# Kernel optimization log

Hardware: AMD Instinct MI355X
Metric: run time of the kernel (lower is better)

The kernel has to match this reference:

```python
import jax, jax.numpy as jnp
import numpy as np

D = 1024      # latent_dimension
NH = 8        # num_heads
ND = 256      # drug num_functions
NT = 128      # target num_functions
B = 128       # batch
EPS_LN = 1e-5
EPS_COS = 1e-8


def _proj_attend(x, W, b, in_w, in_b, out_w, out_b, g, beta):
    """ParallelFcWithAttention.forward: per-feature Linear(1,D)+ReLU, MHSA, LN, sum.
    x: (B, >=F); W,b: (F, D); in_w: (3D, D); out_w: (D, D); g,beta: (D,)."""
    F = W.shape[0]
    # fused batched scale+bias+ReLU replacing the Python loop of Linear(1,D)
    h = jax.nn.relu(x[:, :F, None] * W[None] + b[None])           # (B, F, D)
    Bsz = h.shape[0]
    qkv = h @ in_w.T + in_b                                       # (B, F, 3D)
    q, k, v = jnp.split(qkv, 3, axis=-1)
    Dh = D // NH
    def split_heads(t):
        return t.reshape(Bsz, F, NH, Dh).transpose(0, 2, 1, 3)   # (B, H, F, Dh)
    q, k, v = split_heads(q), split_heads(k), split_heads(v)
    scale = np.float32(1.0 / np.sqrt(Dh))
    scores = jnp.einsum('bhqd,bhkd->bhqk', q, k) * scale          # (B, H, F, F)
    attn = jax.nn.softmax(scores, axis=-1)
    o = jnp.einsum('bhqk,bhkd->bhqd', attn, v)                    # (B, H, F, Dh)
    o = o.transpose(0, 2, 1, 3).reshape(Bsz, F, D)
    o = o @ out_w.T + out_b
    mu = o.mean(axis=-1, keepdims=True)
    var = ((o - mu) ** 2).mean(axis=-1, keepdims=True)
    o = (o - mu) / jnp.sqrt(var + EPS_LN) * g + beta              # LayerNorm
    return o.sum(axis=1)                                          # (B, D)


def setup_inputs() -> dict:
    key = jax.random.key(0)
    ks = jax.random.split(key, 20)
    s = np.float32(0.02)
    inp = {
        'drug':    jax.random.normal(ks[0], (B, 2048), jnp.float32),
        'target':  jax.random.normal(ks[1], (B, 1024), jnp.float32),
        'dW':      jax.random.normal(ks[2], (ND, D), jnp.float32) * s,
        'db':      jax.random.normal(ks[3], (ND, D), jnp.float32) * s,
        'd_in_w':  jax.random.normal(ks[4], (3 * D, D), jnp.float32) * s,
        'd_in_b':  jnp.zeros((3 * D,), jnp.float32),
        'd_out_w': jax.random.normal(ks[5], (D, D), jnp.float32) * s,
        'd_out_b': jnp.zeros((D,), jnp.float32),
        'd_g':     jnp.ones((D,), jnp.float32),
        'd_beta':  jnp.zeros((D,), jnp.float32),
        'tW':      jax.random.normal(ks[6], (NT, D), jnp.float32) * s,
        'tb':      jax.random.normal(ks[7], (NT, D), jnp.float32) * s,
        't_in_w':  jax.random.normal(ks[8], (3 * D, D), jnp.float32) * s,
        't_in_b':  jnp.zeros((3 * D,), jnp.float32),
        't_out_w': jax.random.normal(ks[9], (D, D), jnp.float32) * s,
        't_out_b': jnp.zeros((D,), jnp.float32),
        't_g':     jnp.ones((D,), jnp.float32),
        't_beta':  jnp.zeros((D,), jnp.float32),
    }
    return inp


def reference(drug, target, dW, db, d_in_w, d_in_b, d_out_w, d_out_b, d_g, d_beta,
              tW, tb, t_in_w, t_in_b, t_out_w, t_out_b, t_g, t_beta):
    dp = _proj_attend(drug, dW, db, d_in_w, d_in_b, d_out_w, d_out_b, d_g, d_beta)   # (B, D)
    tp = _proj_attend(target, tW, tb, t_in_w, t_in_b, t_out_w, t_out_b, t_g, t_beta) # (B, D)
    # Cosine similarity over latent dim (torch CosineSimilarity dim=1), then sigmoid
    dot = jnp.sum(dp * tp, axis=-1)
    denom = jnp.maximum(jnp.linalg.norm(dp, axis=-1) * jnp.linalg.norm(tp, axis=-1), EPS_COS)
    return jax.nn.sigmoid(dot / denom)                                               # (B,)
```

## Files before the change

kernel.cpp:

```cpp
#include <hip/hip_runtime.h>

typedef unsigned short u16;
typedef unsigned int   u32;
typedef unsigned char  u8;

using bf16x8 = __attribute__((ext_vector_type(8))) short;
using f32x4  = __attribute__((ext_vector_type(4))) float;
using i32x4  = __attribute__((ext_vector_type(4))) int;

__device__ __forceinline__ float bf2f(u16 h) {
  u32 u = ((u32)h) << 16;
  return __builtin_bit_cast(float, u);
}
__device__ __forceinline__ u16 f2bf(float f) {
  u32 u = __builtin_bit_cast(u32, f);
  u += 0x7fffu + ((u >> 16) & 1u);
  return (u16)(u >> 16);
}

__device__ __forceinline__ void gload16(const void* src, void* ldsdst) {
  __builtin_amdgcn_global_load_lds(
      (const __attribute__((address_space(1))) void*)src,
      (__attribute__((address_space(3))) void*)ldsdst, 16, 0, 0);
}

__device__ __forceinline__ void mfma_i8(i32x4& c, i32x4 a, i32x4 b) {
  asm volatile("v_mfma_i32_16x16x64_i8 %0, %1, %2, %0" : "+a"(c) : "v"(a), "v"(b));
}

__device__ __forceinline__ int xcd_swz(int wg, int nwg) {
  int q = nwg >> 3, r = nwg & 7, xcd = wg & 7, loc = wg >> 3;
  return (xcd < r ? xcd * (q + 1) : r * (q + 1) + (xcd - r) * q) + loc;
}

__global__ __launch_bounds__(256) void cvt_bf16(const float* __restrict__ in,
                                                u16* __restrict__ out, int n8) {
  int i = blockIdx.x * 256 + threadIdx.x;
  if (i >= n8) return;
  const float* p = in + (size_t)i * 8;
  bf16x8 o;
#pragma unroll
  for (int j = 0; j < 8; ++j) o[j] = (short)f2bf(p[j]);
  *(bf16x8*)(out + (size_t)i * 8) = o;
}

__global__ __launch_bounds__(256) void cvt_w_i8(const float* __restrict__ in,
                                                u8* __restrict__ out,
                                                float* __restrict__ sc) {
  const int row  = blockIdx.x * 4 + (threadIdx.x >> 6);
  const int lane = threadIdx.x & 63;
  const float4* p = (const float4*)(in + (size_t)row * 1024 + lane * 16);
  float v[16];
  float mx = 0.f;
#pragma unroll
  for (int i = 0; i < 4; ++i) {
    float4 t = p[i];
    v[i * 4 + 0] = t.x; v[i * 4 + 1] = t.y; v[i * 4 + 2] = t.z; v[i * 4 + 3] = t.w;
#pragma unroll
    for (int j = 0; j < 4; ++j) mx = fmaxf(mx, fabsf(v[i * 4 + j]));
  }
#pragma unroll
  for (int m = 1; m < 64; m <<= 1) mx = fmaxf(mx, __shfl_xor(mx, m));
  const float scale = mx > 0.f ? 127.f / mx : 0.f;
  u32 pk[4];
#pragma unroll
  for (int i = 0; i < 4; ++i) {
    u32 b0 = (u32)(__float2int_rn(v[i * 4 + 0] * scale) & 0xff);
    u32 b1 = (u32)(__float2int_rn(v[i * 4 + 1] * scale) & 0xff);
    u32 b2 = (u32)(__float2int_rn(v[i * 4 + 2] * scale) & 0xff);
    u32 b3 = (u32)(__float2int_rn(v[i * 4 + 3] * scale) & 0xff);
    pk[i] = b0 | (b1 << 8) | (b2 << 16) | (b3 << 24);
  }
  *(uint4*)(out + (size_t)row * 1024 + lane * 16) = make_uint4(pk[0], pk[1], pk[2], pk[3]);
  if (lane == 0) sc[row] = mx > 0.f ? mx / 127.f : 0.f;
}

__global__ __launch_bounds__(256) void hgen_i8(const float* __restrict__ x,
                                               const float* __restrict__ W,
                                               const float* __restrict__ bias,
                                               u8* __restrict__ h, float* __restrict__ hsc,
                                               int F, int logF, int b0, int xstride) {
  const int row  = blockIdx.x * 4 + (threadIdx.x >> 6);
  const int lane = threadIdx.x & 63;
  const int f = row & (F - 1);
  const int b = b0 + (row >> logF);
  const float xv = x[(size_t)b * xstride + f];
  const float4* wp = (const float4*)(W + (size_t)f * 1024 + lane * 16);
  const float4* bp = (const float4*)(bias + (size_t)f * 1024 + lane * 16);
  float hv[16];
  float mx = 0.f;
#pragma unroll
  for (int i = 0; i < 4; ++i) {
    float4 wv = wp[i];
    float4 bv = bp[i];
    hv[i * 4 + 0] = fmaxf(xv * wv.x + bv.x, 0.f);
    hv[i * 4 + 1] = fmaxf(xv * wv.y + bv.y, 0.f);
    hv[i * 4 + 2] = fmaxf(xv * wv.z + bv.z, 0.f);
    hv[i * 4 + 3] = fmaxf(xv * wv.w + bv.w, 0.f);
#pragma unroll
    for (int j = 0; j < 4; ++j) mx = fmaxf(mx, hv[i * 4 + j]);
  }
#pragma unroll
  for (int m = 1; m < 64; m <<= 1) mx = fmaxf(mx, __shfl_xor(mx, m));
  const float scale = mx > 0.f ? 127.f / mx : 0.f;
  u32 pk[4];
#pragma unroll
  for (int i = 0; i < 4; ++i) {
    u32 q0 = (u32)__float2int_rn(hv[i * 4 + 0] * scale);
    u32 q1 = (u32)__float2int_rn(hv[i * 4 + 1] * scale);
    u32 q2 = (u32)__float2int_rn(hv[i * 4 + 2] * scale);
    u32 q3 = (u32)__float2int_rn(hv[i * 4 + 3] * scale);
    pk[i] = q0 | (q1 << 8) | (q2 << 16) | (q3 << 24);
  }
  *(uint4*)(h + (size_t)row * 1024 + lane * 16) = make_uint4(pk[0], pk[1], pk[2], pk[3]);
  if (lane == 0) hsc[row] = mx > 0.f ? mx / 127.f : 0.f;
}

__global__ __launch_bounds__(512, 4) void gemm_i8(const u8* __restrict__ A,
                                                  const u8* __restrict__ B,
                                                  const float* __restrict__ sAsc,
                                                  const float* __restrict__ sBsc,
                                                  const float* __restrict__ bias,
                                                  u16* __restrict__ C,
                                                  int M, int N, int K) {
  __shared__ u8 sA[3][256 * 64];
  __shared__ u8 sB[3][128 * 64];
  const int tid  = threadIdx.x;
  const int lane = tid & 63;
  const int w    = tid >> 6;
  const int wm   = w >> 1;
  const int wn   = w & 1;

  const int nwg = gridDim.x * gridDim.y;
  const int wg  = blockIdx.y * gridDim.x + blockIdx.x;
  const int swz = xcd_swz(wg, nwg);
  const int n0 = (swz % gridDim.x) * 128;
  const int m0 = (swz / gridDim.x) * 256;

  i32x4 acc[4][4] = {};

  const int r_in  = lane >> 2;
  const int s_src = (lane & 3) ^ ((lane >> 3) & 3);

  auto stage = [&](int kt, int b) {
    const int k0 = kt << 6;
    gload16(A + (size_t)(m0 + w * 16 + r_in) * K + k0 + s_src * 16, &sA[b][w * 1024]);
    gload16(A + (size_t)(m0 + (w + 8) * 16 + r_in) * K + k0 + s_src * 16, &sA[b][(w + 8) * 1024]);
    gload16(B + (size_t)(n0 + w * 16 + r_in) * K + k0 + s_src * 16, &sB[b][w * 1024]);
  };

  const int NT = K >> 6;
  stage(0, 0);
  stage(1, 1);
  asm volatile("s_waitcnt vmcnt(3)" ::: "memory");
  __builtin_amdgcn_s_barrier();

  int cur = 0, nx = 2;
  for (int t = 0; t < NT; ++t) {
    const bool more = (t + 2 < NT);
    if (more) stage(t + 2, nx);

    i32x4 af[4], bg[4];
    const int g = lane >> 4;
#pragma unroll
    for (int mf = 0; mf < 4; ++mf) {
      int ra = wm * 64 + mf * 16 + (lane & 15);
      af[mf] = *(const i32x4*)(&sA[cur][ra * 64 + ((g ^ ((ra >> 1) & 3)) * 16)]);
    }
#pragma unroll
    for (int nf = 0; nf < 4; ++nf) {
      int rb = wn * 64 + nf * 16 + (lane & 15);
      bg[nf] = *(const i32x4*)(&sB[cur][rb * 64 + ((g ^ ((rb >> 1) & 3)) * 16)]);
    }
    asm volatile("s_waitcnt lgkmcnt(0)" ::: "memory");
    __builtin_amdgcn_sched_barrier(0);
    __builtin_amdgcn_s_setprio(1);
#pragma unroll
    for (int mf = 0; mf < 4; ++mf)
#pragma unroll
      for (int nf = 0; nf < 4; ++nf)
        mfma_i8(acc[mf][nf], af[mf], bg[nf]);
    __builtin_amdgcn_s_setprio(0);
    if (more) asm volatile("s_waitcnt vmcnt(3)" ::: "memory");
    else      asm volatile("s_waitcnt vmcnt(0)" ::: "memory");
    __builtin_amdgcn_s_barrier();
    cur = (cur == 2) ? 0 : cur + 1;
    nx  = (nx  == 2) ? 0 : nx  + 1;
  }

#pragma unroll
  for (int nf = 0; nf < 4; ++nf) {
    int cl = n0 + wn * 64 + nf * 16 + (lane & 15);
    float sb  = sBsc[cl];
    float bsv = bias[cl];
#pragma unroll
    for (int mf = 0; mf < 4; ++mf) {
      int r0 = m0 + wm * 64 + mf * 16 + (lane >> 4) * 4;
      float4 sa4 = *(const float4*)(sAsc + r0);
      const float* sap = (const float*)&sa4;
#pragma unroll
      for (int reg = 0; reg < 4; ++reg)
        C[(size_t)(r0 + reg) * N + cl] =
            f2bf((float)acc[mf][nf][reg] * (sap[reg] * sb) + bsv);
    }
  }
}

__global__ __launch_bounds__(512, 4) void gemm_ph(const u16* __restrict__ A,
                                                  const u16* __restrict__ B,
                                                  const float* __restrict__ bias,
                                                  u16* __restrict__ C,
                                                  int M, int N, int K) {
  __shared__ u16 sA[3][256 * 32];
  __shared__ u16 sB[3][128 * 32];
  const int tid  = threadIdx.x;
  const int lane = tid & 63;
  const int w    = tid >> 6;
  const int wm   = w >> 1;
  const int wn   = w & 1;

  const int nwg = gridDim.x * gridDim.y;
  const int wg  = blockIdx.y * gridDim.x + blockIdx.x;
  const int swz = xcd_swz(wg, nwg);
  const int n0 = (swz % gridDim.x) * 128;
  const int m0 = (swz / gridDim.x) * 256;

  f32x4 acc[4][4] = {};

  const int r_in  = lane >> 2;
  const int s_src = (lane & 3) ^ ((lane >> 3) & 3);

  auto stage = [&](int kt, int b) {
    const int k0 = kt << 5;
    gload16(A + (size_t)(m0 + w * 16 + r_in) * K + k0 + s_src * 8, &sA[b][w * 512]);
    gload16(A + (size_t)(m0 + (w + 8) * 16 + r_in) * K + k0 + s_src * 8, &sA[b][(w + 8) * 512]);
    gload16(B + (size_t)(n0 + w * 16 + r_in) * K + k0 + s_src * 8, &sB[b][w * 512]);
  };

  const int NT = K >> 5;
  stage(0, 0);
  stage(1, 1);
  asm volatile("s_waitcnt vmcnt(3)" ::: "memory");
  __builtin_amdgcn_s_barrier();

  int cur = 0, nx = 2;
  for (int t = 0; t < NT; ++t) {
    const bool more = (t + 2 < NT);
    if (more) stage(t + 2, nx);

    bf16x8 af[4], bg[4];
    const int g = lane >> 4;
#pragma unroll
    for (int mf = 0; mf < 4; ++mf) {
      int ra = wm * 64 + mf * 16 + (lane & 15);
      af[mf] = *(const bf16x8*)(&sA[cur][ra * 32 + ((g ^ ((ra >> 1) & 3)) * 8)]);
    }
#pragma unroll
    for (int nf = 0; nf < 4; ++nf) {
      int rb = wn * 64 + nf * 16 + (lane & 15);
      bg[nf] = *(const bf16x8*)(&sB[cur][rb * 32 + ((g ^ ((rb >> 1) & 3)) * 8)]);
    }
    asm volatile("s_waitcnt lgkmcnt(0)" ::: "memory");
    __builtin_amdgcn_sched_barrier(0);
    __builtin_amdgcn_s_setprio(1);
#pragma unroll
    for (int mf = 0; mf < 4; ++mf)
#pragma unroll
      for (int nf = 0; nf < 4; ++nf)
        acc[mf][nf] = __builtin_amdgcn_mfma_f32_16x16x32_bf16(af[mf], bg[nf], acc[mf][nf], 0, 0, 0);
    __builtin_amdgcn_s_setprio(0);
    if (more) asm volatile("s_waitcnt vmcnt(3)" ::: "memory");
    else      asm volatile("s_waitcnt vmcnt(0)" ::: "memory");
    __builtin_amdgcn_s_barrier();
    cur = (cur == 2) ? 0 : cur + 1;
    nx  = (nx  == 2) ? 0 : nx  + 1;
  }

#pragma unroll
  for (int nf = 0; nf < 4; ++nf) {
    int cl = n0 + wn * 64 + nf * 16 + (lane & 15);
    float bsv = bias[cl];
#pragma unroll
    for (int mf = 0; mf < 4; ++mf) {
      int r0 = m0 + wm * 64 + mf * 16 + (lane >> 4) * 4;
#pragma unroll
      for (int reg = 0; reg < 4; ++reg)
        C[(size_t)(r0 + reg) * N + cl] = f2bf(acc[mf][nf][reg] + bsv);
    }
  }
}

__global__ __launch_bounds__(512) void attn(const u16* __restrict__ qkv,
                                            u16* __restrict__ o_out, int F) {
  __shared__ u16 q_lds[128 * 136];
  __shared__ u16 k_lds[64 * 136];
  __shared__ u16 vT[128 * 72];
  __shared__ u16 p_lds[8 * 16 * 72];

  const int tid  = threadIdx.x;
  const int lane = tid & 63;
  const int w    = tid >> 6;

  const int swzb = xcd_swz(blockIdx.x, gridDim.x);
  const int nqb  = F >> 7;
  const int qb   = swzb % nqb;
  const int head = (swzb / nqb) & 7;
  const int bc   = swzb / (nqb * 8);

  const size_t rowbase = (size_t)bc * F * 3072;
  const float scale = 0.08838834764831845f;

  {
    const u16* qsrc = qkv + rowbase + (size_t)(qb * 128) * 3072 + head * 128;
    for (int it = tid; it < 2048; it += 512) {
      int r = it >> 4, s = it & 15;
      bf16x8 v = *(const bf16x8*)(qsrc + (size_t)r * 3072 + s * 8);
      bf16x8 o;
#pragma unroll
      for (int j = 0; j < 8; ++j) o[j] = (short)f2bf(bf2f((u16)v[j]) * scale);
      *(bf16x8*)(q_lds + r * 136 + s * 8) = o;
    }
  }

  f32x4 o_acc[8] = {};
  float m_run = -INFINITY, l_run = 0.f;
  const int qr = lane & 15;
  const int g4 = lane >> 4;

  const int nkb = F >> 6;
  for (int kb = 0; kb < nkb; ++kb) {
    __syncthreads();
    const u16* ksrc = qkv + rowbase + (size_t)(kb * 64) * 3072 + 1024 + head * 128;
    const u16* vsrc = ksrc + 1024;
    for (int it = tid; it < 1024; it += 512) {
      int r = it >> 4, s = it & 15;
      *(bf16x8*)(k_lds + r * 136 + s * 8) = *(const bf16x8*)(ksrc + (size_t)r * 3072 + s * 8);
    }
    {
      int g2 = tid >> 4, s = tid & 15;
      const u16* v0 = vsrc + (size_t)(2 * g2) * 3072 + s * 8;
      bf16x8 a = *(const bf16x8*)(v0);
      bf16x8 b = *(const bf16x8*)(v0 + 3072);
      int rs0 = (2 * g2) ^ ((s & 7) << 3);
      int d0  = s * 8;
#pragma unroll
      for (int j = 0; j < 8; ++j) {
        u32 pk = (u32)(u16)a[j] | ((u32)(u16)b[j] << 16);
        *(u32*)(vT + (d0 + j) * 72 + rs0) = pk;
      }
    }
    __syncthreads();

    f32x4 sa[4] = {};
#pragma unroll
    for (int kk = 0; kk < 4; ++kk) {
      bf16x8 bq = *(const bf16x8*)(q_lds + (w * 16 + qr) * 136 + kk * 32 + 8 * g4);
#pragma unroll
      for (int f = 0; f < 4; ++f) {
        bf16x8 ak = *(const bf16x8*)(k_lds + (f * 16 + qr) * 136 + kk * 32 + 8 * g4);
        sa[f] = __builtin_amdgcn_mfma_f32_16x16x32_bf16(ak, bq, sa[f], 0, 0, 0);
      }
    }

    float tmax = -INFINITY;
#pragma unroll
    for (int f = 0; f < 4; ++f)
#pragma unroll
      for (int rr = 0; rr < 4; ++rr) tmax = fmaxf(tmax, sa[f][rr]);
    tmax = fmaxf(tmax, __shfl_xor(tmax, 16));
    tmax = fmaxf(tmax, __shfl_xor(tmax, 32));
    float mnew  = fmaxf(m_run, tmax);
    float alpha = __expf(m_run - mnew);
    float psum  = 0.f;
#pragma unroll
    for (int f = 0; f < 4; ++f) {
      u16 pp[4];
#pragma unroll
      for (int rr = 0; rr < 4; ++rr) {
        float p = __expf(sa[f][rr] - mnew);
        psum += p;
        pp[rr] = f2bf(p);
      }
      uint2 u;
      u.x = (u32)pp[0] | ((u32)pp[1] << 16);
      u.y = (u32)pp[2] | ((u32)pp[3] << 16);
      *(uint2*)(p_lds + w * 1152 + qr * 72 + f * 16 + g4 * 4) = u;
    }
    psum += __shfl_xor(psum, 16);
    psum += __shfl_xor(psum, 32);
    l_run = l_run * alpha + psum;
    m_run = mnew;

#pragma unroll
    for (int rr = 0; rr < 4; ++rr) {
      float ar = __shfl(alpha, g4 * 4 + rr);
#pragma unroll
      for (int g = 0; g < 8; ++g) o_acc[g][rr] *= ar;
    }

#pragma unroll
    for (int kk2 = 0; kk2 < 2; ++kk2) {
      bf16x8 pa = *(const bf16x8*)(p_lds + w * 1152 + qr * 72 + kk2 * 32 + 8 * g4);
#pragma unroll
      for (int g = 0; g < 8; ++g) {
        int swv = ((g * 2 + (qr >> 3)) & 7) << 3;
        bf16x8 vb = *(const bf16x8*)(vT + (g * 16 + qr) * 72 + ((kk2 * 32 + 8 * g4) ^ swv));
        o_acc[g] = __builtin_amdgcn_mfma_f32_16x16x32_bf16(pa, vb, o_acc[g], 0, 0, 0);
      }
    }
  }

  float linv = 1.f / l_run;
#pragma unroll
  for (int rr = 0; rr < 4; ++rr) {
    float lr = __shfl(linv, g4 * 4 + rr);
    size_t row = (size_t)bc * F + qb * 128 + w * 16 + g4 * 4 + rr;
#pragma unroll
    for (int g = 0; g < 8; ++g)
      o_out[row * 1024 + head * 128 + g * 16 + qr] = f2bf(o_acc[g][rr] * lr);
  }
}

__global__ __launch_bounds__(256) void ln_stats(const u16* __restrict__ proj,
                                                float2* __restrict__ stats) {
  int row  = blockIdx.x * 4 + (threadIdx.x >> 6);
  int lane = threadIdx.x & 63;
  const u16* p = proj + (size_t)row * 1024;
  float s = 0.f, s2 = 0.f;
#pragma unroll
  for (int i = 0; i < 2; ++i) {
    bf16x8 v = *(const bf16x8*)(p + (lane + i * 64) * 8);
#pragma unroll
    for (int j = 0; j < 8; ++j) { float f = bf2f((u16)v[j]); s += f; s2 += f * f; }
  }
#pragma unroll
  for (int m = 1; m < 64; m <<= 1) { s += __shfl_xor(s, m); s2 += __shfl_xor(s2, m); }
  if (lane == 0) {
    float mu  = s * (1.f / 1024.f);
    float var = s2 * (1.f / 1024.f) - mu * mu;
    stats[row] = make_float2(mu, rsqrtf(var + 1e-5f));
  }
}

__global__ __launch_bounds__(256) void ln_accum(const u16* __restrict__ proj,
                                                const float2* __restrict__ stats,
                                                const float* __restrict__ g,
                                                const float* __restrict__ beta,
                                                float* __restrict__ dp, int F, int b0) {
  int d  = blockIdx.x * 256 + threadIdx.x;
  int bc = blockIdx.z;
  int f0 = blockIdx.y * 64;
  const u16* base = proj + ((size_t)(bc * F + f0)) * 1024 + d;
  const float2* st = stats + bc * F + f0;
  float acc = 0.f;
  for (int f = 0; f < 64; ++f) {
    float2 s = st[f];
    acc += (bf2f(base[(size_t)f * 1024]) - s.x) * s.y;
  }
  acc = acc * g[d] + 64.f * beta[d];
  atomicAdd(&dp[(size_t)(b0 + bc) * 1024 + d], acc);
}

__global__ __launch_bounds__(256) void cosine_sig(const float* __restrict__ dp,
                                                  const float* __restrict__ tp,
                                                  float* __restrict__ out) {
  __shared__ float red[3][4];
  int b = blockIdx.x;
  int tid = threadIdx.x, lane = tid & 63, w = tid >> 6;
  float dot = 0.f, n1 = 0.f, n2 = 0.f;
  for (int i = tid; i < 1024; i += 256) {
    float a = dp[(size_t)b * 1024 + i], c = tp[(size_t)b * 1024 + i];
    dot += a * c; n1 += a * a; n2 += c * c;
  }
#pragma unroll
  for (int m = 1; m < 64; m <<= 1) {
    dot += __shfl_xor(dot, m); n1 += __shfl_xor(n1, m); n2 += __shfl_xor(n2, m);
  }
  if (lane == 0) { red[0][w] = dot; red[1][w] = n1; red[2][w] = n2; }
  __syncthreads();
  if (tid == 0) {
    dot = red[0][0] + red[0][1] + red[0][2] + red[0][3];
    n1  = red[1][0] + red[1][1] + red[1][2] + red[1][3];
    n2  = red[2][0] + red[2][1] + red[2][2] + red[2][3];
    float denom = fmaxf(sqrtf(n1) * sqrtf(n2), 1e-8f);
    out[b] = 1.f / (1.f + __expf(-dot / denom));
  }
}

extern "C" void kernel_launch(void* const* d_in, const int* in_sizes, int n_in,
                              void* d_out, int out_size, void* d_ws, size_t ws_size,
                              hipStream_t stream) {
  const float* drug   = (const float*)d_in[0];
  const float* target = (const float*)d_in[1];

  char* p = (char*)d_ws;
  auto alloc = [&](size_t bytes) -> char* {
    char* r = p; p += (bytes + 255) & ~(size_t)255; return r;
  };

  u8*    w8_d   = (u8*)alloc((size_t)3072 * 1024);
  float* wsc_d  = (float*)alloc((size_t)3072 * 4);
  u8*    w8_t   = (u8*)alloc((size_t)3072 * 1024);
  float* wsc_t  = (float*)alloc((size_t)3072 * 4);
  u16*   w_out_d = (u16*)alloc((size_t)1024 * 1024 * 2);
  u16*   w_out_t = (u16*)alloc((size_t)1024 * 1024 * 2);
  float* dp    = (float*)alloc((size_t)2 * 128 * 1024 * 4);
  float* tp    = dp + 128 * 1024;

  size_t fixed = (size_t)(p - (char*)d_ws);
  size_t per = (size_t)256 * 1024
             + (size_t)256 * 4
             + (size_t)256 * 3072 * 2
             + (size_t)256 * 1024 * 2 * 2
             + (size_t)256 * 8 + 4096;
  int Bc = 8;
  if      (fixed + 128 * per <= ws_size) Bc = 128;
  else if (fixed +  64 * per <= ws_size) Bc = 64;
  else if (fixed +  32 * per <= ws_size) Bc = 32;
  else if (fixed +  16 * per <= ws_size) Bc = 16;

  u8*    h8     = (u8*)alloc((size_t)Bc * 256 * 1024);
  float* hsc    = (float*)alloc((size_t)Bc * 256 * 4);
  u16*   qkvbuf = (u16*)alloc((size_t)Bc * 256 * 3072 * 2);
  u16*   obuf   = (u16*)alloc((size_t)Bc * 256 * 1024 * 2);
  u16*   projbuf= (u16*)alloc((size_t)Bc * 256 * 1024 * 2);
  float2* statsb = (float2*)alloc((size_t)Bc * 256 * 8);

  cvt_w_i8<<<768, 256, 0, stream>>>((const float*)d_in[4],  w8_d, wsc_d);
  cvt_w_i8<<<768, 256, 0, stream>>>((const float*)d_in[12], w8_t, wsc_t);
  cvt_bf16<<<512, 256, 0, stream>>>((const float*)d_in[6],  w_out_d, 1024 * 128);
  cvt_bf16<<<512, 256, 0, stream>>>((const float*)d_in[14], w_out_t, 1024 * 128);
  hipMemsetAsync(dp, 0, (size_t)2 * 128 * 1024 * 4, stream);

  for (int br = 0; br < 2; ++br) {
    const int F = br ? 128 : 256, logF = br ? 7 : 8, xstride = br ? 1024 : 2048;
    const float* x    = br ? target : drug;
    const float* W    = (const float*)d_in[br ? 10 : 2];
    const float* Wb   = (const float*)d_in[br ? 11 : 3];
    u8*          w8   = br ? w8_t : w8_d;
    float*       wsc  = br ? wsc_t : wsc_d;
    const float* inb  = (const float*)d_in[br ? 13 : 5];
    u16*         wout = br ? w_out_t : w_out_d;
    const float* outb = (const float*)d_in[br ? 15 : 7];
    const float* gg   = (const float*)d_in[br ? 16 : 8];
    const float* bb   = (const float*)d_in[br ? 17 : 9];
    float*       accp = br ? tp : dp;

    const int nb = (br ? (2 * Bc > 128 ? 128 : 2 * Bc) : (Bc > 128 ? 128 : Bc));

    for (int b0 = 0; b0 < 128; b0 += nb) {
      const int Mr = nb * F;
      hgen_i8<<<Mr / 4, 256, 0, stream>>>(x, W, Wb, h8, hsc, F, logF, b0, xstride);
      gemm_i8<<<dim3(3072 / 128, Mr / 256), 512, 0, stream>>>(h8, w8, hsc, wsc, inb, qkvbuf, Mr, 3072, 1024);
      attn<<<(F / 128) * 8 * nb, 512, 0, stream>>>(qkvbuf, obuf, F);
      gemm_ph<<<dim3(1024 / 128, Mr / 256), 512, 0, stream>>>(obuf, wout, outb, projbuf, Mr, 1024, 1024);
      ln_stats<<<Mr / 4, 256, 0, stream>>>(projbuf, statsb);
      ln_accum<<<dim3(4, F / 64, nb), 256, 0, stream>>>(projbuf, statsb, gg, bb, accp, F, b0);
    }
  }
  cosine_sig<<<128, 256, 0, stream>>>(dp, tp, (float*)d_out);
}
```

Measured before the change: 618.9 us.

## Quantize out-projection to int8 GEMM and keep Q fragments in registers

```diff
diff --git a/kernel.cpp b/kernel.cpp
--- a/kernel.cpp
+++ b/kernel.cpp
@@ -31,17 +31,6 @@
 __device__ __forceinline__ int xcd_swz(int wg, int nwg) {
   int q = nwg >> 3, r = nwg & 7, xcd = wg & 7, loc = wg >> 3;
   return (xcd < r ? xcd * (q + 1) : r * (q + 1) + (xcd - r) * q) + loc;
-}
-
-__global__ __launch_bounds__(256) void cvt_bf16(const float* __restrict__ in,
-                                                u16* __restrict__ out, int n8) {
-  int i = blockIdx.x * 256 + threadIdx.x;
-  if (i >= n8) return;
-  const float* p = in + (size_t)i * 8;
-  bf16x8 o;
-#pragma unroll
-  for (int j = 0; j < 8; ++j) o[j] = (short)f2bf(p[j]);
-  *(bf16x8*)(out + (size_t)i * 8) = o;
 }
 
 __global__ __launch_bounds__(256) void cvt_w_i8(const float* __restrict__ in,
@@ -58,6 +47,40 @@
     v[i * 4 + 0] = t.x; v[i * 4 + 1] = t.y; v[i * 4 + 2] = t.z; v[i * 4 + 3] = t.w;
 #pragma unroll
     for (int j = 0; j < 4; ++j) mx = fmaxf(mx, fabsf(v[i * 4 + j]));
+  }
+#pragma unroll
+  for (int m = 1; m < 64; m <<= 1) mx = fmaxf(mx, __shfl_xor(mx, m));
+  const float scale = mx > 0.f ? 127.f / mx : 0.f;
+  u32 pk[4];
+#pragma unroll
+  for (int i = 0; i < 4; ++i) {
+    u32 b0 = (u32)(__float2int_rn(v[i * 4 + 0] * scale) & 0xff);
+    u32 b1 = (u32)(__float2int_rn(v[i * 4 + 1] * scale) & 0xff);
+    u32 b2 = (u32)(__float2int_rn(v[i * 4 + 2] * scale) & 0xff);
+    u32 b3 = (u32)(__float2int_rn(v[i * 4 + 3] * scale) & 0xff);
+    pk[i] = b0 | (b1 << 8) | (b2 << 16) | (b3 << 24);
+  }
+  *(uint4*)(out + (size_t)row * 1024 + lane * 16) = make_uint4(pk[0], pk[1], pk[2], pk[3]);
+  if (lane == 0) sc[row] = mx > 0.f ? mx / 127.f : 0.f;
+}
+
+__global__ __launch_bounds__(256) void quant_i8(const u16* __restrict__ in,
+                                                u8* __restrict__ out,
+                                                float* __restrict__ sc) {
+  const int row  = blockIdx.x * 4 + (threadIdx.x >> 6);
+  const int lane = threadIdx.x & 63;
+  const u16* p = in + (size_t)row * 1024 + lane * 16;
+  float v[16];
+  float mx = 0.f;
+#pragma unroll
+  for (int i = 0; i < 2; ++i) {
+    bf16x8 t = *(const bf16x8*)(p + i * 8);
+#pragma unroll
+    for (int j = 0; j < 8; ++j) {
+      float f = bf2f((u16)t[j]);
+      v[i * 8 + j] = f;
+      mx = fmaxf(mx, fabsf(f));
+    }
   }
 #pragma unroll
   for (int m = 1; m < 64; m <<= 1) mx = fmaxf(mx, __shfl_xor(mx, m));
@@ -206,93 +229,8 @@
   }
 }
 
-__global__ __launch_bounds__(512, 4) void gemm_ph(const u16* __restrict__ A,
-                                                  const u16* __restrict__ B,
-                                                  const float* __restrict__ bias,
-                                                  u16* __restrict__ C,
-                                                  int M, int N, int K) {
-  __shared__ u16 sA[3][256 * 32];
-  __shared__ u16 sB[3][128 * 32];
-  const int tid  = threadIdx.x;
-  const int lane = tid & 63;
-  const int w    = tid >> 6;
-  const int wm   = w >> 1;
-  const int wn   = w & 1;
-
-  const int nwg = gridDim.x * gridDim.y;
-  const int wg  = blockIdx.y * gridDim.x + blockIdx.x;
-  const int swz = xcd_swz(wg, nwg);
-  const int n0 = (swz % gridDim.x) * 128;
-  const int m0 = (swz / gridDim.x) * 256;
-
-  f32x4 acc[4][4] = {};
-
-  const int r_in  = lane >> 2;
-  const int s_src = (lane & 3) ^ ((lane >> 3) & 3);
-
-  auto stage = [&](int kt, int b) {
-    const int k0 = kt << 5;
-    gload16(A + (size_t)(m0 + w * 16 + r_in) * K + k0 + s_src * 8, &sA[b][w * 512]);
-    gload16(A + (size_t)(m0 + (w + 8) * 16 + r_in) * K + k0 + s_src * 8, &sA[b][(w + 8) * 512]);
-    gload16(B + (size_t)(n0 + w * 16 + r_in) * K + k0 + s_src * 8, &sB[b][w * 512]);
-  };
-
-  const int NT = K >> 5;
-  stage(0, 0);
-  stage(1, 1);
-  asm volatile("s_waitcnt vmcnt(3)" ::: "memory");
-  __builtin_amdgcn_s_barrier();
-
-  int cur = 0, nx = 2;
-  for (int t = 0; t < NT; ++t) {
-    const bool more = (t + 2 < NT);
-    if (more) stage(t + 2, nx);
-
-    bf16x8 af[4], bg[4];
-    const int g = lane >> 4;
-#pragma unroll
-    for (int mf = 0; mf < 4; ++mf) {
-      int ra = wm * 64 + mf * 16 + (lane & 15);
-      af[mf] = *(const bf16x8*)(&sA[cur][ra * 32 + ((g ^ ((ra >> 1) & 3)) * 8)]);
-    }
-#pragma unroll
-    for (int nf = 0; nf < 4; ++nf) {
-      int rb = wn * 64 + nf * 16 + (lane & 15);
-      bg[nf] = *(const bf16x8*)(&sB[cur][rb * 32 + ((g ^ ((rb >> 1) & 3)) * 8)]);
-    }
-    asm volatile("s_waitcnt lgkmcnt(0)" ::: "memory");
-    __builtin_amdgcn_sched_barrier(0);
-    __builtin_amdgcn_s_setprio(1);
-#pragma unroll
-    for (int mf = 0; mf < 4; ++mf)
-#pragma unroll
-      for (int nf = 0; nf < 4; ++nf)
-        acc[mf][nf] = __builtin_amdgcn_mfma_f32_16x16x32_bf16(af[mf], bg[nf], acc[mf][nf], 0, 0, 0);
-    __builtin_amdgcn_s_setprio(0);
-    if (more) asm volatile("s_waitcnt vmcnt(3)" ::: "memory");
-    else      asm volatile("s_waitcnt vmcnt(0)" ::: "memory");
-    __builtin_amdgcn_s_barrier();
-    cur = (cur == 2) ? 0 : cur + 1;
-    nx  = (nx  == 2) ? 0 : nx  + 1;
-  }
-
-#pragma unroll
-  for (int nf = 0; nf < 4; ++nf) {
-    int cl = n0 + wn * 64 + nf * 16 + (lane & 15);
-    float bsv = bias[cl];
-#pragma unroll
-    for (int mf = 0; mf < 4; ++mf) {
-      int r0 = m0 + wm * 64 + mf * 16 + (lane >> 4) * 4;
-#pragma unroll
-      for (int reg = 0; reg < 4; ++reg)
-        C[(size_t)(r0 + reg) * N + cl] = f2bf(acc[mf][nf][reg] + bsv);
-    }
-  }
-}
-
-__global__ __launch_bounds__(512) void attn(const u16* __restrict__ qkv,
-                                            u16* __restrict__ o_out, int F) {
-  __shared__ u16 q_lds[128 * 136];
+__global__ __launch_bounds__(512, 4) void attn(const u16* __restrict__ qkv,
+                                               u16* __restrict__ o_out, int F) {
   __shared__ u16 k_lds[64 * 136];
   __shared__ u16 vT[128 * 72];
   __shared__ u16 p_lds[8 * 16 * 72];
@@ -310,22 +248,24 @@
   const size_t rowbase = (size_t)bc * F * 3072;
   const float scale = 0.08838834764831845f;
 
+  const int qr = lane & 15;
+  const int g4 = lane >> 4;
+
+  bf16x8 qreg[4];
   {
-    const u16* qsrc = qkv + rowbase + (size_t)(qb * 128) * 3072 + head * 128;
-    for (int it = tid; it < 2048; it += 512) {
-      int r = it >> 4, s = it & 15;
-      bf16x8 v = *(const bf16x8*)(qsrc + (size_t)r * 3072 + s * 8);
-      bf16x8 o;
-#pragma unroll
-      for (int j = 0; j < 8; ++j) o[j] = (short)f2bf(bf2f((u16)v[j]) * scale);
-      *(bf16x8*)(q_lds + r * 136 + s * 8) = o;
+    const u16* qsrc = qkv + rowbase +
+                      (size_t)(qb * 128 + w * 16 + qr) * 3072 + head * 128;
+#pragma unroll
+    for (int kk = 0; kk < 4; ++kk) {
+      bf16x8 v = *(const bf16x8*)(qsrc + kk * 32 + 8 * g4);
+#pragma unroll
+      for (int j = 0; j < 8; ++j) v[j] = (short)f2bf(bf2f((u16)v[j]) * scale);
+      qreg[kk] = v;
     }
   }
 
   f32x4 o_acc[8] = {};
   float m_run = -INFINITY, l_run = 0.f;
-  const int qr = lane & 15;
-  const int g4 = lane >> 4;
 
   const int nkb = F >> 6;
   for (int kb = 0; kb < nkb; ++kb) {
@@ -354,11 +294,10 @@
     f32x4 sa[4] = {};
 #pragma unroll
     for (int kk = 0; kk < 4; ++kk) {
-      bf16x8 bq = *(const bf16x8*)(q_lds + (w * 16 + qr) * 136 + kk * 32 + 8 * g4);
 #pragma unroll
       for (int f = 0; f < 4; ++f) {
         bf16x8 ak = *(const bf16x8*)(k_lds + (f * 16 + qr) * 136 + kk * 32 + 8 * g4);
-        sa[f] = __builtin_amdgcn_mfma_f32_16x16x32_bf16(ak, bq, sa[f], 0, 0, 0);
+        sa[f] = __builtin_amdgcn_mfma_f32_16x16x32_bf16(ak, qreg[kk], sa[f], 0, 0, 0);
       }
     }
 
@@ -498,14 +437,16 @@
     char* r = p; p += (bytes + 255) & ~(size_t)255; return r;
   };
 
-  u8*    w8_d   = (u8*)alloc((size_t)3072 * 1024);
-  float* wsc_d  = (float*)alloc((size_t)3072 * 4);
-  u8*    w8_t   = (u8*)alloc((size_t)3072 * 1024);
-  float* wsc_t  = (float*)alloc((size_t)3072 * 4);
-  u16*   w_out_d = (u16*)alloc((size_t)1024 * 1024 * 2);
-  u16*   w_out_t = (u16*)alloc((size_t)1024 * 1024 * 2);
-  float* dp    = (float*)alloc((size_t)2 * 128 * 1024 * 4);
-  float* tp    = dp + 128 * 1024;
+  u8*    w8_d    = (u8*)alloc((size_t)3072 * 1024);
+  float* wsc_d   = (float*)alloc((size_t)3072 * 4);
+  u8*    w8_t    = (u8*)alloc((size_t)3072 * 1024);
+  float* wsc_t   = (float*)alloc((size_t)3072 * 4);
+  u8*    w8o_d   = (u8*)alloc((size_t)1024 * 1024);
+  float* wsco_d  = (float*)alloc((size_t)1024 * 4);
+  u8*    w8o_t   = (u8*)alloc((size_t)1024 * 1024);
+  float* wsco_t  = (float*)alloc((size_t)1024 * 4);
+  float* dp      = (float*)alloc((size_t)2 * 128 * 1024 * 4);
+  float* tp      = dp + 128 * 1024;
 
   size_t fixed = (size_t)(p - (char*)d_ws);
   size_t per = (size_t)256 * 1024
@@ -528,8 +469,8 @@
 
   cvt_w_i8<<<768, 256, 0, stream>>>((const float*)d_in[4],  w8_d, wsc_d);
   cvt_w_i8<<<768, 256, 0, stream>>>((const float*)d_in[12], w8_t, wsc_t);
-  cvt_bf16<<<512, 256, 0, stream>>>((const float*)d_in[6],  w_out_d, 1024 * 128);
-  cvt_bf16<<<512, 256, 0, stream>>>((const float*)d_in[14], w_out_t, 1024 * 128);
+  cvt_w_i8<<<256, 256, 0, stream>>>((const float*)d_in[6],  w8o_d, wsco_d);
+  cvt_w_i8<<<256, 256, 0, stream>>>((const float*)d_in[14], w8o_t, wsco_t);
   hipMemsetAsync(dp, 0, (size_t)2 * 128 * 1024 * 4, stream);
 
   for (int br = 0; br < 2; ++br) {
@@ -540,7 +481,8 @@
     u8*          w8   = br ? w8_t : w8_d;
     float*       wsc  = br ? wsc_t : wsc_d;
     const float* inb  = (const float*)d_in[br ? 13 : 5];
-    u16*         wout = br ? w_out_t : w_out_d;
+    u8*          w8o  = br ? w8o_t : w8o_d;
+    float*       wsco = br ? wsco_t : wsco_d;
     const float* outb = (const float*)d_in[br ? 15 : 7];
     const float* gg   = (const float*)d_in[br ? 16 : 8];
     const float* bb   = (const float*)d_in[br ? 17 : 9];
@@ -553,7 +495,8 @@
       hgen_i8<<<Mr / 4, 256, 0, stream>>>(x, W, Wb, h8, hsc, F, logF, b0, xstride);
       gemm_i8<<<dim3(3072 / 128, Mr / 256), 512, 0, stream>>>(h8, w8, hsc, wsc, inb, qkvbuf, Mr, 3072, 1024);
       attn<<<(F / 128) * 8 * nb, 512, 0, stream>>>(qkvbuf, obuf, F);
-      gemm_ph<<<dim3(1024 / 128, Mr / 256), 512, 0, stream>>>(obuf, wout, outb, projbuf, Mr, 1024, 1024);
+      quant_i8<<<Mr / 4, 256, 0, stream>>>(obuf, h8, hsc);
+      gemm_i8<<<dim3(1024 / 128, Mr / 256), 512, 0, stream>>>(h8, w8o, hsc, wsco, outb, projbuf, Mr, 1024, 1024);
       ln_stats<<<Mr / 4, 256, 0, stream>>>(projbuf, statsb);
       ln_accum<<<dim3(4, F / 64, nb), 256, 0, stream>>>(projbuf, statsb, gg, bb, accp, F, b0);
     }
```

After: 579.7 us. 6.3% less time.
